# Kernel optimization log

Hardware: AMD Instinct MI355X
Metric: run time of the kernel (lower is better)

## Reference

```python
import jax, jax.numpy as jnp
import numpy as np

B = 131072
NUM_MODS = 6
NUM_PREDS = 30
CLS_TH = 2.0
CLS_IGNORE = 0.2
MGN = 0.2
CLS_COEF = 1.0
REG_COEF = 1.0


def setup_inputs() -> dict:
    key = jax.random.key(0)
    k1, k2, k3 = jax.random.split(key, 3)
    reg = jax.random.normal(k1, (B, NUM_MODS, NUM_PREDS, 2), jnp.float32)
    cls = jax.random.normal(k2, (B, NUM_MODS), jnp.float32)
    gt_preds = jax.random.normal(k3, (B, NUM_PREDS, 2), jnp.float32)
    has_preds = jnp.ones((B, NUM_PREDS), dtype=bool)
    return {"reg": reg, "cls": cls, "gt_preds": gt_preds, "has_preds": has_preds}


def _loss(reg, cls, gt, has):
    # ---------------- PredLoss (LaneGCN cls + reg loss) ----------------
    hasf = has.astype(jnp.float32)
    last = hasf + 0.1 * jnp.arange(NUM_PREDS, dtype=jnp.float32) / float(NUM_PREDS)
    last_idcs = jnp.argmax(last, axis=1)                      # [B]
    max_last = jnp.max(last, axis=1)
    valid = max_last > 1.0                                    # [B] rows kept by `mask`

    # distance of each mode's last-valid point to gt last-valid point
    reg_last = jnp.take_along_axis(reg, last_idcs[:, None, None, None], axis=2)[:, :, 0, :]  # [B,6,2]
    gt_last = jnp.take_along_axis(gt, last_idcs[:, None, None], axis=1)[:, 0, :]             # [B,2]
    dist = jnp.sqrt(((reg_last - gt_last[:, None, :]) ** 2).sum(-1))                          # [B,6]

    min_idcs = jnp.argmin(dist, axis=1)                       # [B]
    min_dist = jnp.min(dist, axis=1)

    cls_min = jnp.take_along_axis(cls, min_idcs[:, None], axis=1)  # [B,1]
    mgn = cls_min - cls                                            # [B,6]
    m01 = (min_dist < CLS_TH)[:, None] & ((dist - min_dist[:, None]) > CLS_IGNORE) & valid[:, None]
    cls_mask = m01 & (mgn < MGN)
    num_cls = cls_mask.sum()
    cls_loss = CLS_COEF * (MGN * num_cls.astype(jnp.float32) - jnp.where(cls_mask, mgn, 0.0).sum())

    # SmoothL1 (beta=1, reduction='sum') over best mode, masked by has & valid
    reg_best = jnp.take_along_axis(reg, min_idcs[:, None, None, None], axis=1)[:, 0]  # [B,30,2]
    diff = reg_best - gt
    ad = jnp.abs(diff)
    sl1 = jnp.where(ad < 1.0, 0.5 * diff * diff, ad - 0.5)
    w = (has & valid[:, None]).astype(jnp.float32)[..., None]  # [B,30,1]
    reg_loss = REG_COEF * (sl1 * w).sum()
    num_reg = (has & valid[:, None]).sum()

    loss = cls_loss / (num_cls.astype(jnp.float32) + 1e-10) + reg_loss / (num_reg.astype(jnp.float32) + 1e-10)

    # ---------------- heading (vectorized over scenes) ----------------
    gx, gy = gt[..., 0], gt[..., 1]                           # [B,30]
    fwd = jnp.arctan2(gy[:, 2:] - gy[:, 1:-1], gx[:, 2:] - gx[:, 1:-1])   # [B,28]
    bwd = jnp.arctan2(gy[:, 1:-1] - gy[:, :-2], gx[:, 1:-1] - gx[:, :-2]) # [B,28]
    head_tmp = jnp.rad2deg(fwd) + jnp.rad2deg(bwd)                         # [B,28]
    mid = jnp.where((fwd == 0.0) | (bwd == 0.0), head_tmp, head_tmp / 2.0)
    head0 = jnp.rad2deg(jnp.arctan2(gy[:, 1] - gy[:, 0], gx[:, 1] - gx[:, 0]))
    headL = jnp.rad2deg(jnp.arctan2(gy[:, -1] - gy[:, -2], gx[:, -1] - gx[:, -2]))
    head = jnp.concatenate([head0[:, None], mid, headL[:, None]], axis=1)  # [B,30]
    moving = jnp.sqrt(((gt[:, 0, :] - gt[:, -1, :]) ** 2).sum(-1)) > 2.0
    head = jnp.where(moving[:, None], head, 0.0)

    # ---------------- rotated dist_error (per-timestep 2x2 rotation) ----------------
    de0 = jnp.abs(gt[:, None, :, :] - reg)                    # [B,6,30,2] L1Loss(reduction='none')
    theta = jnp.deg2rad(-head)                                # [B,30]
    c = jnp.cos(theta)[:, None, :]                            # [B,1,30]
    s = jnp.sin(theta)[:, None, :]
    dx, dy = de0[..., 0], de0[..., 1]                         # [B,6,30]
    rx = c * dx - s * dy
    ry = s * dx + c * dy
    de = jnp.abs(jnp.stack([rx, ry], axis=-1))                # [B,6,30,2]

    top1 = jnp.argmax(cls, axis=1)                            # [B]
    de_top = jnp.take_along_axis(de, top1[:, None, None, None], axis=1)[:, 0]  # [B,30,2]

    ade6_x = de[..., 0].sum(); ade6_y = de[..., 1].sum()
    fde6_x = de[:, :, -1, 0].sum(); fde6_y = de[:, :, -1, 1].sum()
    ade1_x = de_top[..., 0].sum(); ade1_y = de_top[..., 1].sum()
    fde1_x = de_top[:, -1, 0].sum(); fde1_y = de_top[:, -1, 1].sum()

    Bn = de.shape[0]
    counts = jnp.array([
        NUM_MODS * Bn * NUM_PREDS,  # ade6_num
        NUM_MODS * Bn,              # fde6_num
        Bn * NUM_PREDS,             # ade1_num
        Bn,                         # fde1_num
    ], dtype=jnp.float32)

    return jnp.stack([
        loss, cls_loss, num_cls.astype(jnp.float32), reg_loss, num_reg.astype(jnp.float32),
        ade6_x, ade6_y, fde6_x, fde6_y, counts[0], counts[1],
        ade1_x, ade1_y, fde1_x, fde1_y, counts[2], counts[3],
    ])


def reference(reg, cls, gt_preds, has_preds):
    return _loss(reg, cls, gt_preds, has_preds)
```

## Files before the change

kernel.cpp:

```cpp
#include <hip/hip_runtime.h>
#include <math.h>

#define NROWS 131072
#define NMODS 6
#define NPREDS 30
#define RPB 16
#define NBLK (NROWS / RPB)
#define ELEMS (RPB * NMODS * 15)

#define ACC_SLOT(ws, i) ((float*)((char*)(ws) + (size_t)(i) * 256))

__device__ __forceinline__ float wave_reduce(float v) {
    v += __shfl_xor(v, 32);
    v += __shfl_xor(v, 16);
    v += __shfl_xor(v, 8);
    v += __shfl_xor(v, 4);
    v += __shfl_xor(v, 2);
    v += __shfl_xor(v, 1);
    return v;
}

__global__ __launch_bounds__(256) void loss_fused(
    const float* __restrict__ reg,
    const float* __restrict__ cls,
    const float* __restrict__ gt,
    const int* __restrict__ has,
    void* __restrict__ ws)
{
    const int tid = threadIdx.x;
    const int rb  = blockIdx.x * RPB;

    __shared__ float2 s_gt[RPB * NPREDS];
    __shared__ float2 s_st[RPB * NPREDS];
    __shared__ uint2  s_meta[RPB];
    __shared__ float  s_red[4][12];

    const float4* reg4 = (const float4*)reg + (size_t)rb * 90;
    float4 rv[6];
    #pragma unroll
    for (int i = 0; i < 6; ++i) {
        int k = tid + i * 256;
        if (k < ELEMS) rv[i] = reg4[k];
    }

    if (tid < RPB * NPREDS / 2)
        ((float4*)s_gt)[tid] = ((const float4*)gt)[(size_t)rb * (NPREDS / 2) + tid];
    __syncthreads();

    float acc[12];
    #pragma unroll
    for (int i = 0; i < 12; ++i) acc[i] = 0.f;

    if (tid < RPB) {
        const int r = rb + tid;
        const int2* h2 = (const int2*)(has + (size_t)r * NPREDS);
        unsigned mask = 0u;
        #pragma unroll
        for (int i = 0; i < 15; ++i) {
            int2 h = h2[i];
            mask |= (h.x != 0 ? 1u : 0u) << (2 * i);
            mask |= (h.y != 0 ? 1u : 0u) << (2 * i + 1);
        }
        const int  last  = mask ? (31 - __builtin_clz(mask)) : (NPREDS - 1);
        const bool valid = (mask & ~1u) != 0u;

        float2 gl = s_gt[tid * NPREDS + last];
        const float2* rrow = (const float2*)(reg + (size_t)r * NMODS * NPREDS * 2);
        float dists[NMODS];
        #pragma unroll
        for (int m = 0; m < NMODS; ++m) {
            float2 rl = rrow[m * NPREDS + last];
            float ax = rl.x - gl.x, ay = rl.y - gl.y;
            dists[m] = sqrtf(ax * ax + ay * ay);
        }
        float mind = dists[0]; int mini = 0;
        #pragma unroll
        for (int m = 1; m < NMODS; ++m)
            if (dists[m] < mind) { mind = dists[m]; mini = m; }

        const float2* c2 = (const float2*)(cls + (size_t)r * NMODS);
        float cv[NMODS];
        #pragma unroll
        for (int i = 0; i < 3; ++i) { float2 c = c2[i]; cv[2*i] = c.x; cv[2*i+1] = c.y; }
        float clsmin = cv[0];
        #pragma unroll
        for (int m = 1; m < NMODS; ++m) clsmin = (m == mini) ? cv[m] : clsmin;

        if (valid && (mind < 2.0f)) {
            #pragma unroll
            for (int m = 0; m < NMODS; ++m) {
                float mgn = clsmin - cv[m];
                if (((dists[m] - mind) > 0.2f) && (mgn < 0.2f)) {
                    acc[10] += 1.0f;
                    acc[9]  += mgn;
                }
            }
        }
        float bc = cv[0]; int top1 = 0;
        #pragma unroll
        for (int m = 1; m < NMODS; ++m)
            if (cv[m] > bc) { bc = cv[m]; top1 = m; }

        if (valid) acc[11] += (float)__builtin_popcount(mask);

        s_meta[tid] = make_uint2(mask,
            (unsigned)mini | ((unsigned)top1 << 4) | (valid ? 256u : 0u));
    }

    #pragma unroll
    for (int it = 0; it < 2; ++it) {
        int idx = tid + it * 256;
        if (idx < RPB * NPREDS) {
            int row = idx / NPREDS;
            int t   = idx - row * NPREDS;
            const float2* g = s_gt + row * NPREDS;
            float2 g0 = g[0], g29 = g[NPREDS - 1];
            float mdx = g0.x - g29.x, mdy = g0.y - g29.y;
            bool moving = (mdx * mdx + mdy * mdy) > 4.0f;

            float2 cur = g[t];
            float2 prv = g[(t > 0) ? t - 1 : 0];
            float2 nxt = g[(t < NPREDS - 1) ? t + 1 : NPREDS - 1];
            float fwd = atan2f(nxt.y - cur.y, nxt.x - cur.x);
            float bwd = atan2f(cur.y - prv.y, cur.x - prv.x);
            float head = (t == 0) ? fwd
                       : ((t == NPREDS - 1) ? bwd
                       : ((fwd == 0.f || bwd == 0.f) ? (fwd + bwd)
                                                     : 0.5f * (fwd + bwd)));
            if (!moving) head = 0.f;
            float s, c;
            __sincosf(-head, &s, &c);
            s_st[idx] = make_float2(c, s);
        }
    }
    __syncthreads();

    #pragma unroll
    for (int i = 0; i < 6; ++i) {
        int k = tid + i * 256;
        if (k < ELEMS) {
            int row = k / 90;
            int rem = k - row * 90;
            int m   = rem / 15;
            int q   = rem - m * 15;
            int t0  = 2 * q;

            uint2  mt  = s_meta[row];
            float4 gp  = ((const float4*)s_gt)[row * 15 + q];
            float4 sp  = ((const float4*)s_st)[row * 15 + q];
            float4 v   = rv[i];

            unsigned mini = mt.y & 15u, top1 = (mt.y >> 4) & 15u;
            bool valid  = (mt.y & 256u) != 0u;
            bool isTop  = ((unsigned)m == top1);
            bool isBest = ((unsigned)m == mini) && valid;
            bool is29   = (q == 14);

            {
                float dx = fabsf(gp.x - v.x), dy = fabsf(gp.y - v.y);
                float ax = fabsf(sp.x * dx - sp.y * dy);
                float ay = fabsf(sp.y * dx + sp.x * dy);
                acc[0] += ax; acc[1] += ay;
                if (isTop) { acc[4] += ax; acc[5] += ay; }
                if (isBest && ((mt.x >> t0) & 1u)) {
                    float e0 = v.x - gp.x, e1 = v.y - gp.y;
                    float q0 = fabsf(e0), q1 = fabsf(e1);
                    acc[8] += (q0 < 1.f) ? (0.5f * e0 * e0) : (q0 - 0.5f);
                    acc[8] += (q1 < 1.f) ? (0.5f * e1 * e1) : (q1 - 0.5f);
                }
            }
            {
                float dx = fabsf(gp.z - v.z), dy = fabsf(gp.w - v.w);
                float ax = fabsf(sp.z * dx - sp.w * dy);
                float ay = fabsf(sp.w * dx + sp.z * dy);
                acc[0] += ax; acc[1] += ay;
                if (isTop) { acc[4] += ax; acc[5] += ay; }
                if (is29) {
                    acc[2] += ax; acc[3] += ay;
                    if (isTop) { acc[6] += ax; acc[7] += ay; }
                }
                if (isBest && ((mt.x >> (t0 + 1)) & 1u)) {
                    float e0 = v.z - gp.z, e1 = v.w - gp.w;
                    float q0 = fabsf(e0), q1 = fabsf(e1);
                    acc[8] += (q0 < 1.f) ? (0.5f * e0 * e0) : (q0 - 0.5f);
                    acc[8] += (q1 < 1.f) ? (0.5f * e1 * e1) : (q1 - 0.5f);
                }
            }
        }
    }

    #pragma unroll
    for (int i = 0; i < 12; ++i) acc[i] = wave_reduce(acc[i]);

    const int lane = tid & 63;
    const int wid  = tid >> 6;
    if (lane == 0) {
        #pragma unroll
        for (int i = 0; i < 12; ++i) s_red[wid][i] = acc[i];
    }
    __syncthreads();
    if (tid < 12) {
        float s = s_red[0][tid] + s_red[1][tid] + s_red[2][tid] + s_red[3][tid];
        atomicAdd(ACC_SLOT(ws, tid), s);
    }
}

__global__ void finalize(void* ws, float* __restrict__ out) {
    if (threadIdx.x == 0) {
        float nc = *ACC_SLOT(ws, 10), nr = *ACC_SLOT(ws, 11);
        float cls_loss = 0.2f * nc - *ACC_SLOT(ws, 9);
        float reg_loss = *ACC_SLOT(ws, 8);
        float loss = cls_loss / (nc + 1e-10f) + reg_loss / (nr + 1e-10f);
        out[0]  = loss;
        out[1]  = cls_loss;
        out[2]  = nc;
        out[3]  = reg_loss;
        out[4]  = nr;
        out[5]  = *ACC_SLOT(ws, 0);
        out[6]  = *ACC_SLOT(ws, 1);
        out[7]  = *ACC_SLOT(ws, 2);
        out[8]  = *ACC_SLOT(ws, 3);
        out[9]  = 23592960.0f;
        out[10] = 786432.0f;
        out[11] = *ACC_SLOT(ws, 4);
        out[12] = *ACC_SLOT(ws, 5);
        out[13] = *ACC_SLOT(ws, 6);
        out[14] = *ACC_SLOT(ws, 7);
        out[15] = 3932160.0f;
        out[16] = 131072.0f;
    }
}

extern "C" void kernel_launch(void* const* d_in, const int* in_sizes, int n_in,
                              void* d_out, int out_size, void* d_ws, size_t ws_size,
                              hipStream_t stream) {
    const float* reg = (const float*)d_in[0];
    const float* cls = (const float*)d_in[1];
    const float* gt  = (const float*)d_in[2];
    const int*   has = (const int*)d_in[3];
    float* out = (float*)d_out;

    hipMemsetAsync(d_ws, 0, 4096, stream);
    loss_fused<<<NBLK, 256, 0, stream>>>(reg, cls, gt, has, d_ws);
    finalize<<<1, 64, 0, stream>>>(d_ws, out);
}
```

Baseline: 346.5 us.

## Restructure loss kernel into persistent per-wave groups with ballot masks and no block barriers

Each wavefront now independently processes groups of 4 rows in a grid-stride loop over a fixed 2048-block grid. Block-wide __syncthreads are replaced by wave barriers plus LDS waitcnt. The has-mask is built with ballots and per-row metadata is broadcast via shuffles instead of shared memory. The aim is to remove block-level sync stalls and the serial 16-thread has-loading phase, and to amortise launch and reduction overhead. In exchange each wave has less memory parallelism per iteration, and correctness now depends on the hand-written waitcnt encoding.

```diff
diff --git a/kernel.cpp b/kernel.cpp
--- a/kernel.cpp
+++ b/kernel.cpp
@@ -4,11 +4,19 @@
 #define NROWS 131072
 #define NMODS 6
 #define NPREDS 30
-#define RPB 16
-#define NBLK (NROWS / RPB)
-#define ELEMS (RPB * NMODS * 15)
+#define RPG 4
+#define NGROUPS (NROWS / RPG)
+#define NBLK 2048
+#define NWAVES (NBLK * 4)
+#define GF4 (RPG * NMODS * 15)
 
 #define ACC_SLOT(ws, i) ((float*)((char*)(ws) + (size_t)(i) * 256))
+
+#define LGKM_WAIT() do { \
+    __builtin_amdgcn_wave_barrier(); \
+    __builtin_amdgcn_s_waitcnt(0xC07F); \
+    __builtin_amdgcn_wave_barrier(); \
+} while (0)
 
 __device__ __forceinline__ float wave_reduce(float v) {
     v += __shfl_xor(v, 32);
@@ -20,180 +28,189 @@
     return v;
 }
 
-__global__ __launch_bounds__(256) void loss_fused(
+__global__ __launch_bounds__(256) void loss_wave(
     const float* __restrict__ reg,
     const float* __restrict__ cls,
     const float* __restrict__ gt,
     const int* __restrict__ has,
     void* __restrict__ ws)
 {
-    const int tid = threadIdx.x;
-    const int rb  = blockIdx.x * RPB;
-
-    __shared__ float2 s_gt[RPB * NPREDS];
-    __shared__ float2 s_st[RPB * NPREDS];
-    __shared__ uint2  s_meta[RPB];
+    const int tid  = threadIdx.x;
+    const int lane = tid & 63;
+    const int wid  = tid >> 6;
+    const int gwave = blockIdx.x * 4 + wid;
+
+    __shared__ float2 s_gt[4][RPG * NPREDS];
+    __shared__ float2 s_ct[4][RPG * NPREDS];
     __shared__ float  s_red[4][12];
-
-    const float4* reg4 = (const float4*)reg + (size_t)rb * 90;
-    float4 rv[6];
-    #pragma unroll
-    for (int i = 0; i < 6; ++i) {
-        int k = tid + i * 256;
-        if (k < ELEMS) rv[i] = reg4[k];
-    }
-
-    if (tid < RPB * NPREDS / 2)
-        ((float4*)s_gt)[tid] = ((const float4*)gt)[(size_t)rb * (NPREDS / 2) + tid];
-    __syncthreads();
 
     float acc[12];
     #pragma unroll
     for (int i = 0; i < 12; ++i) acc[i] = 0.f;
 
-    if (tid < RPB) {
-        const int r = rb + tid;
-        const int2* h2 = (const int2*)(has + (size_t)r * NPREDS);
-        unsigned mask = 0u;
-        #pragma unroll
-        for (int i = 0; i < 15; ++i) {
-            int2 h = h2[i];
-            mask |= (h.x != 0 ? 1u : 0u) << (2 * i);
-            mask |= (h.y != 0 ? 1u : 0u) << (2 * i + 1);
+    for (int g = gwave; g < NGROUPS; g += NWAVES) {
+        const int rb = g * RPG;
+
+        float4 gv = make_float4(0.f, 0.f, 0.f, 0.f);
+        if (lane < 60) gv = ((const float4*)gt)[(size_t)rb * 15 + lane];
+        int2 hv = make_int2(0, 0);
+        if (lane < 60) hv = ((const int2*)has)[(size_t)rb * 15 + lane];
+
+        const float4* reg4 = (const float4*)reg + (size_t)rb * 90;
+        float4 rv[6];
+        #pragma unroll
+        for (int i = 0; i < 5; ++i) rv[i] = reg4[lane + 64 * i];
+        if (lane < 40) rv[5] = reg4[lane + 320];
+
+        unsigned long long bx = __ballot(lane < 60 && hv.x != 0);
+        unsigned long long by = __ballot(lane < 60 && hv.y != 0);
+
+        if (lane < 60) ((float4*)s_gt[wid])[lane] = gv;
+        LGKM_WAIT();
+
+        #pragma unroll
+        for (int it = 0; it < 2; ++it) {
+            int idx = lane + it * 64;
+            if (idx < RPG * NPREDS) {
+                int row = idx / NPREDS;
+                int t   = idx - row * NPREDS;
+                const float2* gp = s_gt[wid] + row * NPREDS;
+                float2 g0 = gp[0], g29 = gp[NPREDS - 1];
+                float mdx = g0.x - g29.x, mdy = g0.y - g29.y;
+                bool moving = (mdx * mdx + mdy * mdy) > 4.0f;
+
+                float2 cur = gp[t];
+                float2 prv = gp[(t > 0) ? t - 1 : 0];
+                float2 nxt = gp[(t < NPREDS - 1) ? t + 1 : NPREDS - 1];
+                float fwd = atan2f(nxt.y - cur.y, nxt.x - cur.x);
+                float bwd = atan2f(cur.y - prv.y, cur.x - prv.x);
+                float head = (t == 0) ? fwd
+                           : ((t == NPREDS - 1) ? bwd
+                           : ((fwd == 0.f || bwd == 0.f) ? (fwd + bwd)
+                                                         : 0.5f * (fwd + bwd)));
+                if (!moving) head = 0.f;
+                float s, c;
+                __sincosf(-head, &s, &c);
+                s_ct[wid][idx] = make_float2(c, s);
+            }
         }
-        const int  last  = mask ? (31 - __builtin_clz(mask)) : (NPREDS - 1);
-        const bool valid = (mask & ~1u) != 0u;
-
-        float2 gl = s_gt[tid * NPREDS + last];
-        const float2* rrow = (const float2*)(reg + (size_t)r * NMODS * NPREDS * 2);
-        float dists[NMODS];
-        #pragma unroll
-        for (int m = 0; m < NMODS; ++m) {
-            float2 rl = rrow[m * NPREDS + last];
-            float ax = rl.x - gl.x, ay = rl.y - gl.y;
-            dists[m] = sqrtf(ax * ax + ay * ay);
+
+        unsigned metaval = 0u;
+        if (lane < RPG) {
+            unsigned ex = (unsigned)((bx >> (15 * lane)) & 0x7FFFull);
+            unsigned ey = (unsigned)((by >> (15 * lane)) & 0x7FFFull);
+            int le = ex ? 2 * (31 - __builtin_clz(ex)) : -1;
+            int lo = ey ? 2 * (31 - __builtin_clz(ey)) + 1 : -1;
+            int last = (le > lo) ? le : lo;
+            if (last < 0) last = NPREDS - 1;
+            bool valid = ((ex & ~1u) | ey) != 0u;
+
+            float2 gl = s_gt[wid][lane * NPREDS + last];
+            const float2* rr = (const float2*)reg + (size_t)(rb + lane) * 180;
+            float dists[NMODS];
+            #pragma unroll
+            for (int m = 0; m < NMODS; ++m) {
+                float2 rl = rr[m * NPREDS + last];
+                float ax = rl.x - gl.x, ay = rl.y - gl.y;
+                dists[m] = sqrtf(ax * ax + ay * ay);
+            }
+            float mind = dists[0]; int mini = 0;
+            #pragma unroll
+            for (int m = 1; m < NMODS; ++m)
+                if (dists[m] < mind) { mind = dists[m]; mini = m; }
+
+            const float2* cc = (const float2*)cls + (size_t)(rb + lane) * 3;
+            float cv[NMODS];
+            #pragma unroll
+            for (int i = 0; i < 3; ++i) { float2 c = cc[i]; cv[2*i] = c.x; cv[2*i+1] = c.y; }
+            float clsmin = cv[0];
+            #pragma unroll
+            for (int m = 1; m < NMODS; ++m) clsmin = (m == mini) ? cv[m] : clsmin;
+
+            if (valid && (mind < 2.0f)) {
+                #pragma unroll
+                for (int m = 0; m < NMODS; ++m) {
+                    float mgn = clsmin - cv[m];
+                    if (((dists[m] - mind) > 0.2f) && (mgn < 0.2f)) {
+                        acc[10] += 1.0f;
+                        acc[9]  += mgn;
+                    }
+                }
+            }
+            float bc = cv[0]; int top1 = 0;
+            #pragma unroll
+            for (int m = 1; m < NMODS; ++m)
+                if (cv[m] > bc) { bc = cv[m]; top1 = m; }
+
+            if (valid)
+                acc[11] += (float)(__builtin_popcount(ex) + __builtin_popcount(ey));
+
+            metaval = (unsigned)mini | ((unsigned)top1 << 4) | (valid ? 256u : 0u);
         }
-        float mind = dists[0]; int mini = 0;
-        #pragma unroll
-        for (int m = 1; m < NMODS; ++m)
-            if (dists[m] < mind) { mind = dists[m]; mini = m; }
-
-        const float2* c2 = (const float2*)(cls + (size_t)r * NMODS);
-        float cv[NMODS];
-        #pragma unroll
-        for (int i = 0; i < 3; ++i) { float2 c = c2[i]; cv[2*i] = c.x; cv[2*i+1] = c.y; }
-        float clsmin = cv[0];
-        #pragma unroll
-        for (int m = 1; m < NMODS; ++m) clsmin = (m == mini) ? cv[m] : clsmin;
-
-        if (valid && (mind < 2.0f)) {
-            #pragma unroll
-            for (int m = 0; m < NMODS; ++m) {
-                float mgn = clsmin - cv[m];
-                if (((dists[m] - mind) > 0.2f) && (mgn < 0.2f)) {
-                    acc[10] += 1.0f;
-                    acc[9]  += mgn;
-                }
-            }
-        }
-        float bc = cv[0]; int top1 = 0;
-        #pragma unroll
-        for (int m = 1; m < NMODS; ++m)
-            if (cv[m] > bc) { bc = cv[m]; top1 = m; }
-
-        if (valid) acc[11] += (float)__builtin_popcount(mask);
-
-        s_meta[tid] = make_uint2(mask,
-            (unsigned)mini | ((unsigned)top1 << 4) | (valid ? 256u : 0u));
-    }
-
-    #pragma unroll
-    for (int it = 0; it < 2; ++it) {
-        int idx = tid + it * 256;
-        if (idx < RPB * NPREDS) {
-            int row = idx / NPREDS;
-            int t   = idx - row * NPREDS;
-            const float2* g = s_gt + row * NPREDS;
-            float2 g0 = g[0], g29 = g[NPREDS - 1];
-            float mdx = g0.x - g29.x, mdy = g0.y - g29.y;
-            bool moving = (mdx * mdx + mdy * mdy) > 4.0f;
-
-            float2 cur = g[t];
-            float2 prv = g[(t > 0) ? t - 1 : 0];
-            float2 nxt = g[(t < NPREDS - 1) ? t + 1 : NPREDS - 1];
-            float fwd = atan2f(nxt.y - cur.y, nxt.x - cur.x);
-            float bwd = atan2f(cur.y - prv.y, cur.x - prv.x);
-            float head = (t == 0) ? fwd
-                       : ((t == NPREDS - 1) ? bwd
-                       : ((fwd == 0.f || bwd == 0.f) ? (fwd + bwd)
-                                                     : 0.5f * (fwd + bwd)));
-            if (!moving) head = 0.f;
-            float s, c;
-            __sincosf(-head, &s, &c);
-            s_st[idx] = make_float2(c, s);
-        }
-    }
-    __syncthreads();
-
-    #pragma unroll
-    for (int i = 0; i < 6; ++i) {
-        int k = tid + i * 256;
-        if (k < ELEMS) {
-            int row = k / 90;
-            int rem = k - row * 90;
+        LGKM_WAIT();
+
+        #pragma unroll
+        for (int i = 0; i < 6; ++i) {
+            int k = lane + 64 * i;
+            bool act = (i < 5) || (lane < 40);
+            int kk = act ? k : 0;
+            int row = kk / 90;
+            int rem = kk - row * 90;
             int m   = rem / 15;
-            int q   = rem - m * 15;
+            int q   = rem - 15 * m;
             int t0  = 2 * q;
 
-            uint2  mt  = s_meta[row];
-            float4 gp  = ((const float4*)s_gt)[row * 15 + q];
-            float4 sp  = ((const float4*)s_st)[row * 15 + q];
-            float4 v   = rv[i];
-
-            unsigned mini = mt.y & 15u, top1 = (mt.y >> 4) & 15u;
-            bool valid  = (mt.y & 256u) != 0u;
+            unsigned mv = (unsigned)__shfl((int)metaval, row);
+            unsigned ex = (unsigned)((bx >> (15 * row)) & 0x7FFFull);
+            unsigned ey = (unsigned)((by >> (15 * row)) & 0x7FFFull);
+            float4 gp = ((const float4*)s_gt[wid])[row * 15 + q];
+            float4 sp = ((const float4*)s_ct[wid])[row * 15 + q];
+            float4 v  = rv[i];
+
+            unsigned mini = mv & 15u, top1 = (mv >> 4) & 15u;
+            bool valid  = (mv & 256u) != 0u;
             bool isTop  = ((unsigned)m == top1);
             bool isBest = ((unsigned)m == mini) && valid;
-            bool is29   = (q == 14);
-
-            {
-                float dx = fabsf(gp.x - v.x), dy = fabsf(gp.y - v.y);
-                float ax = fabsf(sp.x * dx - sp.y * dy);
-                float ay = fabsf(sp.y * dx + sp.x * dy);
-                acc[0] += ax; acc[1] += ay;
-                if (isTop) { acc[4] += ax; acc[5] += ay; }
-                if (isBest && ((mt.x >> t0) & 1u)) {
-                    float e0 = v.x - gp.x, e1 = v.y - gp.y;
-                    float q0 = fabsf(e0), q1 = fabsf(e1);
-                    acc[8] += (q0 < 1.f) ? (0.5f * e0 * e0) : (q0 - 0.5f);
-                    acc[8] += (q1 < 1.f) ? (0.5f * e1 * e1) : (q1 - 0.5f);
+
+            if (act) {
+                {
+                    float dx = fabsf(gp.x - v.x), dy = fabsf(gp.y - v.y);
+                    float ax = fabsf(sp.x * dx - sp.y * dy);
+                    float ay = fabsf(sp.y * dx + sp.x * dy);
+                    acc[0] += ax; acc[1] += ay;
+                    if (isTop) { acc[4] += ax; acc[5] += ay; }
+                    if (isBest && ((ex >> q) & 1u)) {
+                        float e0 = v.x - gp.x, e1 = v.y - gp.y;
+                        float q0 = fabsf(e0), q1 = fabsf(e1);
+                        acc[8] += (q0 < 1.f) ? (0.5f * e0 * e0) : (q0 - 0.5f);
+                        acc[8] += (q1 < 1.f) ? (0.5f * e1 * e1) : (q1 - 0.5f);
+                    }
                 }
-            }
-            {
-                float dx = fabsf(gp.z - v.z), dy = fabsf(gp.w - v.w);
-                float ax = fabsf(sp.z * dx - sp.w * dy);
-                float ay = fabsf(sp.w * dx + sp.z * dy);
-                acc[0] += ax; acc[1] += ay;
-                if (isTop) { acc[4] += ax; acc[5] += ay; }
-                if (is29) {
-                    acc[2] += ax; acc[3] += ay;
-                    if (isTop) { acc[6] += ax; acc[7] += ay; }
+                {
+                    float dx = fabsf(gp.z - v.z), dy = fabsf(gp.w - v.w);
+                    float ax = fabsf(sp.z * dx - sp.w * dy);
+                    float ay = fabsf(sp.w * dx + sp.z * dy);
+                    acc[0] += ax; acc[1] += ay;
+                    if (isTop) { acc[4] += ax; acc[5] += ay; }
+                    if (q == 14) {
+                        acc[2] += ax; acc[3] += ay;
+                        if (isTop) { acc[6] += ax; acc[7] += ay; }
+                    }
+                    if (isBest && ((ey >> q) & 1u)) {
+                        float e0 = v.z - gp.z, e1 = v.w - gp.w;
+                        float q0 = fabsf(e0), q1 = fabsf(e1);
+                        acc[8] += (q0 < 1.f) ? (0.5f * e0 * e0) : (q0 - 0.5f);
+                        acc[8] += (q1 < 1.f) ? (0.5f * e1 * e1) : (q1 - 0.5f);
+                    }
                 }
-                if (isBest && ((mt.x >> (t0 + 1)) & 1u)) {
-                    float e0 = v.z - gp.z, e1 = v.w - gp.w;
-                    float q0 = fabsf(e0), q1 = fabsf(e1);
-                    acc[8] += (q0 < 1.f) ? (0.5f * e0 * e0) : (q0 - 0.5f);
-                    acc[8] += (q1 < 1.f) ? (0.5f * e1 * e1) : (q1 - 0.5f);
-                }
             }
         }
+        __builtin_amdgcn_wave_barrier();
     }
 
     #pragma unroll
     for (int i = 0; i < 12; ++i) acc[i] = wave_reduce(acc[i]);
 
-    const int lane = tid & 63;
-    const int wid  = tid >> 6;
     if (lane == 0) {
         #pragma unroll
         for (int i = 0; i < 12; ++i) s_red[wid][i] = acc[i];
@@ -241,6 +258,6 @@
     float* out = (float*)d_out;
 
     hipMemsetAsync(d_ws, 0, 4096, stream);
-    loss_fused<<<NBLK, 256, 0, stream>>>(reg, cls, gt, has, d_ws);
+    loss_wave<<<NBLK, 256, 0, stream>>>(reg, cls, gt, has, d_ws);
     finalize<<<1, 64, 0, stream>>>(d_ws, out);
 }
```

New measurement: 328.8 us. 5.1% less time.
